# Kernel optimization log

Hardware: AMD Instinct MI355X
Metric: run time of the kernel (lower is better)

## Reference

```python
import jax, jax.numpy as jnp
import numpy as np

N, E, D, C = 40000, 640000, 128, 64


def setup_inputs() -> dict:
    key = jax.random.key(0)
    ks = jax.random.split(key, 12)
    x = jax.random.normal(ks[0], (N, D), dtype=jnp.float32)
    edge_row = jax.random.randint(ks[1], (E,), 0, N, dtype=jnp.int32)
    edge_col = jax.random.randint(ks[2], (E,), 0, N, dtype=jnp.int32)
    edge_val = jax.random.uniform(ks[3], (E,), dtype=jnp.float32)
    s1 = 1.0 / np.sqrt(D)
    W1 = jax.random.uniform(ks[4], (D, D), minval=-s1, maxval=s1, dtype=jnp.float32)
    b1 = jax.random.uniform(ks[5], (D,), minval=-s1, maxval=s1, dtype=jnp.float32)
    W2 = jax.random.uniform(ks[6], (D, D), minval=-s1, maxval=s1, dtype=jnp.float32)
    b2 = jax.random.uniform(ks[7], (D,), minval=-s1, maxval=s1, dtype=jnp.float32)
    Wf = jax.random.uniform(ks[8], (D, C), minval=-s1, maxval=s1, dtype=jnp.float32)
    bf = jax.random.uniform(ks[9], (C,), minval=-s1, maxval=s1, dtype=jnp.float32)
    return {"x": x, "edge_row": edge_row, "edge_col": edge_col, "edge_val": edge_val,
            "W1": W1, "b1": b1, "W2": W2, "b2": b2, "Wf": Wf, "bf": bf}


def _spmm(row, col, val, dense):
    # out[row] += val * dense[col]  == adj @ dense with adj in COO form
    msgs = dense[col] * val[:, None]  # [E, D]
    return jax.ops.segment_sum(msgs, row, num_segments=N)


def reference(x, edge_row, edge_col, edge_val, W1, b1, W2, b2, Wf, bf):
    # gc1: relu(adj @ (x @ W1) + b1)
    h = jax.nn.relu(_spmm(edge_row, edge_col, edge_val, x @ W1) + b1)
    # dropout(p=0.2, training=False) -> identity in eval mode
    # gc2 + residual: relu(adj @ (h @ W2) + b2) + h
    h2 = jax.nn.relu(_spmm(edge_row, edge_col, edge_val, h @ W2) + b2) + h
    # final linear classifier
    return h2 @ Wf + bf
```

## Files before the change

kernel.cpp:

```cpp
#include <hip/hip_runtime.h>

#define N_NODES 40000
#define N_EDGES 640000
#define DIM     128
#define NCLS    64
#define CAP     64

typedef __attribute__((ext_vector_type(8))) short short8v;
typedef __attribute__((ext_vector_type(4))) float f32x4;

__device__ __forceinline__ unsigned short f2bf(float f) {
    unsigned int u = __float_as_uint(f);
    unsigned int r = u + 0x7fffu + ((u >> 16) & 1u);
    return (unsigned short)(r >> 16);
}
__device__ __forceinline__ float bf2f(unsigned int s) {
    return __uint_as_float(s << 16);
}

__global__ void zero_counts(int* __restrict__ counts) {
    int i = blockIdx.x * blockDim.x + threadIdx.x;
    if (i < N_NODES) counts[i] = 0;
}

__global__ void build_bucket(const int* __restrict__ erow, const int* __restrict__ ecol,
                             const float* __restrict__ evalv, int* __restrict__ counts,
                             int* __restrict__ bcol, float* __restrict__ bval) {
    int e = blockIdx.x * blockDim.x + threadIdx.x;
    if (e >= N_EDGES) return;
    int r = erow[e];
    int p = atomicAdd(&counts[r], 1);
    if (p < CAP) {
        bcol[r * CAP + p] = ecol[e];
        bval[r * CAP + p] = evalv[e];
    }
}

__global__ void cast_f32_bf16(const float4* __restrict__ in, uint2* __restrict__ out, int n4) {
    int i = blockIdx.x * blockDim.x + threadIdx.x;
    if (i >= n4) return;
    float4 v = in[i];
    uint2 o;
    o.x = (unsigned)f2bf(v.x) | ((unsigned)f2bf(v.y) << 16);
    o.y = (unsigned)f2bf(v.z) | ((unsigned)f2bf(v.w) << 16);
    out[i] = o;
}

__global__ void wtrans128(const float* __restrict__ W, unsigned short* __restrict__ WT) {
    int e = blockIdx.x * 256 + threadIdx.x;
    int k = e >> 7, n = e & 127;
    WT[n * 128 + k] = f2bf(W[e]);
}
__global__ void wtransF(const float* __restrict__ Wf, unsigned short* __restrict__ WT) {
    int e = blockIdx.x * 256 + threadIdx.x;
    int k = e >> 6, n = e & 63;
    WT[n * 128 + k] = f2bf(Wf[e]);
}

__launch_bounds__(256)
__global__ void gemm_bf16_128(const unsigned short* __restrict__ A,
                              const unsigned short* __restrict__ WT,
                              unsigned short* __restrict__ C) {
    __shared__ unsigned short sB[128 * 128];
    const int tid = threadIdx.x;
    for (int c = tid; c < 2048; c += 256) {
        int n = c >> 4, j = c & 15;
        short8v v = *reinterpret_cast<const short8v*>(WT + n * 128 + 8 * j);
        *reinterpret_cast<short8v*>(&sB[n * 128 + 8 * (j ^ (n & 7))]) = v;
    }
    __syncthreads();

    const int lane = tid & 63;
    const int wv   = tid >> 6;
    const int m0   = blockIdx.x * 64 + wv * 16;
    const int r    = lane & 15;
    const int g    = lane >> 4;

    short8v af[4];
    const unsigned short* arow = A + (size_t)(m0 + r) * 128 + 8 * g;
#pragma unroll
    for (int f = 0; f < 4; ++f)
        af[f] = *reinterpret_cast<const short8v*>(arow + 32 * f);

    f32x4 acc[8];
#pragma unroll
    for (int nt = 0; nt < 8; ++nt) acc[nt] = (f32x4){0.f, 0.f, 0.f, 0.f};

#pragma unroll
    for (int nt = 0; nt < 8; ++nt) {
        const int rw = nt * 16 + r;
        const unsigned short* bbase = &sB[rw * 128];
#pragma unroll
        for (int f = 0; f < 4; ++f) {
            short8v bfr = *reinterpret_cast<const short8v*>(bbase + 8 * ((4 * f + g) ^ (rw & 7)));
            acc[nt] = __builtin_amdgcn_mfma_f32_16x16x32_bf16(af[f], bfr, acc[nt], 0, 0, 0);
        }
    }
#pragma unroll
    for (int nt = 0; nt < 8; ++nt)
#pragma unroll
        for (int rr = 0; rr < 4; ++rr)
            C[(size_t)(m0 + g * 4 + rr) * 128 + nt * 16 + r] = f2bf(acc[nt][rr]);
}

__launch_bounds__(256)
__global__ void gemm_bf16_final(const unsigned short* __restrict__ A,
                                const unsigned short* __restrict__ WT,
                                const float* __restrict__ bias,
                                float* __restrict__ C) {
    __shared__ unsigned short sB[64 * 128];
    const int tid = threadIdx.x;
    for (int c = tid; c < 1024; c += 256) {
        int n = c >> 4, j = c & 15;
        short8v v = *reinterpret_cast<const short8v*>(WT + n * 128 + 8 * j);
        *reinterpret_cast<short8v*>(&sB[n * 128 + 8 * (j ^ (n & 7))]) = v;
    }
    __syncthreads();

    const int lane = tid & 63;
    const int wv   = tid >> 6;
    const int m0   = blockIdx.x * 64 + wv * 16;
    const int r    = lane & 15;
    const int g    = lane >> 4;

    short8v af[4];
    const unsigned short* arow = A + (size_t)(m0 + r) * 128 + 8 * g;
#pragma unroll
    for (int f = 0; f < 4; ++f)
        af[f] = *reinterpret_cast<const short8v*>(arow + 32 * f);

    f32x4 acc[4];
#pragma unroll
    for (int nt = 0; nt < 4; ++nt) acc[nt] = (f32x4){0.f, 0.f, 0.f, 0.f};

#pragma unroll
    for (int nt = 0; nt < 4; ++nt) {
        const int rw = nt * 16 + r;
        const unsigned short* bbase = &sB[rw * 128];
#pragma unroll
        for (int f = 0; f < 4; ++f) {
            short8v bfr = *reinterpret_cast<const short8v*>(bbase + 8 * ((4 * f + g) ^ (rw & 7)));
            acc[nt] = __builtin_amdgcn_mfma_f32_16x16x32_bf16(af[f], bfr, acc[nt], 0, 0, 0);
        }
    }
#pragma unroll
    for (int nt = 0; nt < 4; ++nt)
#pragma unroll
        for (int rr = 0; rr < 4; ++rr)
            C[(size_t)(m0 + g * 4 + rr) * 64 + nt * 16 + r] = acc[nt][rr] + bias[nt * 16 + r];
}

__launch_bounds__(256)
__global__ void spmm_fused_bf16(const unsigned int* __restrict__ dense,
                                const int* __restrict__ bcol, const float* __restrict__ bval,
                                const int* __restrict__ counts,
                                const float* __restrict__ bias,
                                const float* __restrict__ resid,
                                float* __restrict__ out_f32,
                                unsigned int* __restrict__ out_bf) {
    const int lane = threadIdx.x & 63;
    const int wv   = threadIdx.x >> 6;
    const int row  = blockIdx.x * 4 + wv;
    int deg = counts[row];
    if (deg > CAP) deg = CAP;
    const int base = row * CAP;

    int   colr = 0;
    float valr = 0.f;
    if (lane < deg) {
        colr = bcol[base + lane];
        valr = bval[base + lane];
    }
    const int degUp = (deg + 3) & ~3;

    float ax0 = 0.f, ay0 = 0.f, ax1 = 0.f, ay1 = 0.f;
    float ax2 = 0.f, ay2 = 0.f, ax3 = 0.f, ay3 = 0.f;
    for (int i = 0; i < degUp; i += 4) {
        int   c0 = __shfl(colr, i + 0); float v0 = __shfl(valr, i + 0);
        int   c1 = __shfl(colr, i + 1); float v1 = __shfl(valr, i + 1);
        int   c2 = __shfl(colr, i + 2); float v2 = __shfl(valr, i + 2);
        int   c3 = __shfl(colr, i + 3); float v3 = __shfl(valr, i + 3);
        unsigned u0 = dense[(size_t)c0 * 64 + lane];
        unsigned u1 = dense[(size_t)c1 * 64 + lane];
        unsigned u2 = dense[(size_t)c2 * 64 + lane];
        unsigned u3 = dense[(size_t)c3 * 64 + lane];
        ax0 += v0 * bf2f(u0 & 0xffffu); ay0 += v0 * bf2f(u0 >> 16);
        ax1 += v1 * bf2f(u1 & 0xffffu); ay1 += v1 * bf2f(u1 >> 16);
        ax2 += v2 * bf2f(u2 & 0xffffu); ay2 += v2 * bf2f(u2 >> 16);
        ax3 += v3 * bf2f(u3 & 0xffffu); ay3 += v3 * bf2f(u3 >> 16);
    }
    float rx = (ax0 + ax1) + (ax2 + ax3);
    float ry = (ay0 + ay1) + (ay2 + ay3);

    const float2 bb = reinterpret_cast<const float2*>(bias)[lane];
    rx = fmaxf(rx + bb.x, 0.f);
    ry = fmaxf(ry + bb.y, 0.f);
    if (resid) {
        const float2 rr = reinterpret_cast<const float2*>(resid)[(size_t)row * 64 + lane];
        rx += rr.x; ry += rr.y;
    }
    if (out_f32)
        reinterpret_cast<float2*>(out_f32)[(size_t)row * 64 + lane] = make_float2(rx, ry);
    out_bf[(size_t)row * 64 + lane] = (unsigned)f2bf(rx) | ((unsigned)f2bf(ry) << 16);
}

extern "C" void kernel_launch(void* const* d_in, const int* in_sizes, int n_in,
                              void* d_out, int out_size, void* d_ws, size_t ws_size,
                              hipStream_t stream) {
    const float* x    = (const float*)d_in[0];
    const int*   erow = (const int*)  d_in[1];
    const int*   ecol = (const int*)  d_in[2];
    const float* ev   = (const float*)d_in[3];
    const float* W1   = (const float*)d_in[4];
    const float* b1   = (const float*)d_in[5];
    const float* W2   = (const float*)d_in[6];
    const float* b2   = (const float*)d_in[7];
    const float* Wf   = (const float*)d_in[8];
    const float* bf   = (const float*)d_in[9];
    float* out = (float*)d_out;

    char* ws = (char*)d_ws;
    int*   counts = (int*)ws;
    int*   bcol   = (int*)  (ws + 262144);
    float* bval   = (float*)(ws + 262144 + 10485760);
    char*  baseB  = ws + 262144 + 2 * 10485760;
    unsigned short* xb   = (unsigned short*)(baseB);
    unsigned short* gb   = (unsigned short*)(baseB + 1 * 10485760);
    unsigned short* hb   = (unsigned short*)(baseB + 2 * 10485760);
    unsigned short* h2b  = (unsigned short*)(baseB + 3 * 10485760);
    float*          hf   = (float*)        (baseB + 4 * 10485760);
    unsigned short* wt1  = (unsigned short*)(baseB + 6 * 10485760);
    unsigned short* wt2  = (unsigned short*)(baseB + 6 * 10485760 + 65536);
    unsigned short* wtf  = (unsigned short*)(baseB + 6 * 10485760 + 131072);

    zero_counts<<<(N_NODES + 255) / 256, 256, 0, stream>>>(counts);
    build_bucket<<<(N_EDGES + 255) / 256, 256, 0, stream>>>(erow, ecol, ev, counts, bcol, bval);

    cast_f32_bf16<<<(N_NODES * DIM / 4 + 255) / 256, 256, 0, stream>>>(
        (const float4*)x, (uint2*)xb, N_NODES * DIM / 4);
    wtrans128<<<64, 256, 0, stream>>>(W1, wt1);
    wtrans128<<<64, 256, 0, stream>>>(W2, wt2);
    wtransF <<<32, 256, 0, stream>>>(Wf, wtf);

    gemm_bf16_128<<<N_NODES / 64, 256, 0, stream>>>(xb, wt1, gb);
    spmm_fused_bf16<<<N_NODES / 4, 256, 0, stream>>>((const unsigned int*)gb, bcol, bval, counts,
                                                     b1, nullptr, hf, (unsigned int*)hb);
    gemm_bf16_128<<<N_NODES / 64, 256, 0, stream>>>(hb, wt2, gb);
    spmm_fused_bf16<<<N_NODES / 4, 256, 0, stream>>>((const unsigned int*)gb, bcol, bval, counts,
                                                     b2, hf, nullptr, (unsigned int*)h2b);
    gemm_bf16_final<<<N_NODES / 64, 256, 0, stream>>>(h2b, wtf, bf, out);
}
```

Measured before the change: 207.5 us.

## Merge prep kernels, pad atomic counters, and pack col/val into one slot

Folds the cast, counter zeroing and weight transposes into a single launch, which removes several small kernel launches. The per-row counters are padded to a 16-int stride so that atomics on different rows do not share a cache line. Column index and value are stored together as a uint2, so the bucket build does one 8-byte write per edge and the SpMM does one 8-byte read. The padded counters use 16x more memory for counts, and the SpMM reads of deg become strided.

```diff
diff --git a/kernel.cpp b/kernel.cpp
--- a/kernel.cpp
+++ b/kernel.cpp
@@ -5,6 +5,7 @@
 #define DIM     128
 #define NCLS    64
 #define CAP     64
+#define CSTRIDE 16
 
 typedef __attribute__((ext_vector_type(8))) short short8v;
 typedef __attribute__((ext_vector_type(4))) float f32x4;
@@ -18,43 +19,47 @@
     return __uint_as_float(s << 16);
 }
 
-__global__ void zero_counts(int* __restrict__ counts) {
-    int i = blockIdx.x * blockDim.x + threadIdx.x;
-    if (i < N_NODES) counts[i] = 0;
-}
-
+__launch_bounds__(256)
+__global__ void prep(const float4* __restrict__ x4, uint2* __restrict__ xb,
+                     const float* __restrict__ W1, const float* __restrict__ W2,
+                     const float* __restrict__ Wf,
+                     unsigned short* __restrict__ wt1, unsigned short* __restrict__ wt2,
+                     unsigned short* __restrict__ wtf, int* __restrict__ counts) {
+    const int b = blockIdx.x, tid = threadIdx.x;
+    if (b < 5000) {
+        int i = b * 256 + tid;
+        float4 v = x4[i];
+        uint2 o;
+        o.x = (unsigned)f2bf(v.x) | ((unsigned)f2bf(v.y) << 16);
+        o.y = (unsigned)f2bf(v.z) | ((unsigned)f2bf(v.w) << 16);
+        xb[i] = o;
+    } else if (b < 7500) {
+        counts[(b - 5000) * 256 + tid] = 0;
+    } else if (b < 7564) {
+        int e = (b - 7500) * 256 + tid;
+        int k = e >> 7, n = e & 127;
+        wt1[n * 128 + k] = f2bf(W1[e]);
+    } else if (b < 7628) {
+        int e = (b - 7564) * 256 + tid;
+        int k = e >> 7, n = e & 127;
+        wt2[n * 128 + k] = f2bf(W2[e]);
+    } else {
+        int e = (b - 7628) * 256 + tid;
+        int k = e >> 6, n = e & 63;
+        wtf[n * 128 + k] = f2bf(Wf[e]);
+    }
+}
+
+__launch_bounds__(256)
 __global__ void build_bucket(const int* __restrict__ erow, const int* __restrict__ ecol,
                              const float* __restrict__ evalv, int* __restrict__ counts,
-                             int* __restrict__ bcol, float* __restrict__ bval) {
+                             uint2* __restrict__ bslot) {
     int e = blockIdx.x * blockDim.x + threadIdx.x;
     if (e >= N_EDGES) return;
     int r = erow[e];
-    int p = atomicAdd(&counts[r], 1);
-    if (p < CAP) {
-        bcol[r * CAP + p] = ecol[e];
-        bval[r * CAP + p] = evalv[e];
-    }
-}
-
-__global__ void cast_f32_bf16(const float4* __restrict__ in, uint2* __restrict__ out, int n4) {
-    int i = blockIdx.x * blockDim.x + threadIdx.x;
-    if (i >= n4) return;
-    float4 v = in[i];
-    uint2 o;
-    o.x = (unsigned)f2bf(v.x) | ((unsigned)f2bf(v.y) << 16);
-    o.y = (unsigned)f2bf(v.z) | ((unsigned)f2bf(v.w) << 16);
-    out[i] = o;
-}
-
-__global__ void wtrans128(const float* __restrict__ W, unsigned short* __restrict__ WT) {
-    int e = blockIdx.x * 256 + threadIdx.x;
-    int k = e >> 7, n = e & 127;
-    WT[n * 128 + k] = f2bf(W[e]);
-}
-__global__ void wtransF(const float* __restrict__ Wf, unsigned short* __restrict__ WT) {
-    int e = blockIdx.x * 256 + threadIdx.x;
-    int k = e >> 6, n = e & 63;
-    WT[n * 128 + k] = f2bf(Wf[e]);
+    int p = atomicAdd(&counts[r * CSTRIDE], 1);
+    if (p < CAP)
+        bslot[(size_t)r * CAP + p] = make_uint2((unsigned)ecol[e], __float_as_uint(evalv[e]));
 }
 
 __launch_bounds__(256)
@@ -152,7 +157,7 @@
 
 __launch_bounds__(256)
 __global__ void spmm_fused_bf16(const unsigned int* __restrict__ dense,
-                                const int* __restrict__ bcol, const float* __restrict__ bval,
+                                const uint2* __restrict__ bslot,
                                 const int* __restrict__ counts,
                                 const float* __restrict__ bias,
                                 const float* __restrict__ resid,
@@ -161,15 +166,16 @@
     const int lane = threadIdx.x & 63;
     const int wv   = threadIdx.x >> 6;
     const int row  = blockIdx.x * 4 + wv;
-    int deg = counts[row];
+    int deg = counts[row * CSTRIDE];
     if (deg > CAP) deg = CAP;
-    const int base = row * CAP;
+    const size_t base = (size_t)row * CAP;
 
     int   colr = 0;
     float valr = 0.f;
     if (lane < deg) {
-        colr = bcol[base + lane];
-        valr = bval[base + lane];
+        uint2 s = bslot[base + lane];
+        colr = (int)s.x;
+        valr = __uint_as_float(s.y);
     }
     const int degUp = (deg + 3) & ~3;
 
@@ -219,34 +225,28 @@
     const float* bf   = (const float*)d_in[9];
     float* out = (float*)d_out;
 
+    const size_t MB = 1u << 20;
     char* ws = (char*)d_ws;
-    int*   counts = (int*)ws;
-    int*   bcol   = (int*)  (ws + 262144);
-    float* bval   = (float*)(ws + 262144 + 10485760);
-    char*  baseB  = ws + 262144 + 2 * 10485760;
-    unsigned short* xb   = (unsigned short*)(baseB);
-    unsigned short* gb   = (unsigned short*)(baseB + 1 * 10485760);
-    unsigned short* hb   = (unsigned short*)(baseB + 2 * 10485760);
-    unsigned short* h2b  = (unsigned short*)(baseB + 3 * 10485760);
-    float*          hf   = (float*)        (baseB + 4 * 10485760);
-    unsigned short* wt1  = (unsigned short*)(baseB + 6 * 10485760);
-    unsigned short* wt2  = (unsigned short*)(baseB + 6 * 10485760 + 65536);
-    unsigned short* wtf  = (unsigned short*)(baseB + 6 * 10485760 + 131072);
-
-    zero_counts<<<(N_NODES + 255) / 256, 256, 0, stream>>>(counts);
-    build_bucket<<<(N_EDGES + 255) / 256, 256, 0, stream>>>(erow, ecol, ev, counts, bcol, bval);
-
-    cast_f32_bf16<<<(N_NODES * DIM / 4 + 255) / 256, 256, 0, stream>>>(
-        (const float4*)x, (uint2*)xb, N_NODES * DIM / 4);
-    wtrans128<<<64, 256, 0, stream>>>(W1, wt1);
-    wtrans128<<<64, 256, 0, stream>>>(W2, wt2);
-    wtransF <<<32, 256, 0, stream>>>(Wf, wtf);
+    int*            counts = (int*)           (ws + 0 * MB);
+    uint2*          bslot  = (uint2*)         (ws + 4 * MB);
+    unsigned short* xb     = (unsigned short*)(ws + 25 * MB);
+    unsigned short* gb     = (unsigned short*)(ws + 36 * MB);
+    unsigned short* hb     = (unsigned short*)(ws + 47 * MB);
+    unsigned short* h2b    = (unsigned short*)(ws + 58 * MB);
+    float*          hf     = (float*)         (ws + 69 * MB);
+    unsigned short* wt1    = (unsigned short*)(ws + 90 * MB);
+    unsigned short* wt2    = (unsigned short*)(ws + 90 * MB + 65536);
+    unsigned short* wtf    = (unsigned short*)(ws + 90 * MB + 131072);
+
+    prep<<<7660, 256, 0, stream>>>((const float4*)x, (uint2*)xb, W1, W2, Wf,
+                                   wt1, wt2, wtf, counts);
+    build_bucket<<<(N_EDGES + 255) / 256, 256, 0, stream>>>(erow, ecol, ev, counts, bslot);
 
     gemm_bf16_128<<<N_NODES / 64, 256, 0, stream>>>(xb, wt1, gb);
-    spmm_fused_bf16<<<N_NODES / 4, 256, 0, stream>>>((const unsigned int*)gb, bcol, bval, counts,
+    spmm_fused_bf16<<<N_NODES / 4, 256, 0, stream>>>((const unsigned int*)gb, bslot, counts,
                                                      b1, nullptr, hf, (unsigned int*)hb);
     gemm_bf16_128<<<N_NODES / 64, 256, 0, stream>>>(hb, wt2, gb);
-    spmm_fused_bf16<<<N_NODES / 4, 256, 0, stream>>>((const unsigned int*)gb, bcol, bval, counts,
+    spmm_fused_bf16<<<N_NODES / 4, 256, 0, stream>>>((const unsigned int*)gb, bslot, counts,
                                                      b2, hf, nullptr, (unsigned int*)h2b);
     gemm_bf16_final<<<N_NODES / 64, 256, 0, stream>>>(h2b, wtf, bf, out);
 }
```

Measured after the change: 198.1 us. 4.5% less time.
